# Performance work log

Measured on AMD Instinct MI355X. Metric: run time of the kernel, lower is better.

The kernel has to match this reference:

```python
import jax, jax.numpy as jnp
import numpy as np

THRESHOLD = 0.3

def setup_inputs() -> dict:
    key = jax.random.key(0)
    ks = jax.random.split(key, 8)
    B, T, N, d = 4, 32, 1024, 2
    hd, od, hs, osz = 64, 64, 128, 2
    p = lambda k, sh: jax.random.normal(k, sh, jnp.float32) * 0.1
    return {
        "points": jax.random.uniform(ks[0], (B, T, N, d), jnp.float32),
        "W1": p(ks[1], (hd, d)),   "b1": jnp.zeros((hd,), jnp.float32),
        "W2": p(ks[2], (od, hd)),  "b2": jnp.zeros((od,), jnp.float32),
        "Wg": p(ks[3], (hd, od)),  "bg": jnp.zeros((hd,), jnp.float32),
        "Wih": p(ks[4], (3 * hs, hd)), "Whh": p(ks[5], (3 * hs, hs)),
        "bih": jnp.zeros((3 * hs,), jnp.float32), "bhh": jnp.zeros((3 * hs,), jnp.float32),
        "Wf": p(ks[6], (osz, hs)), "bf": jnp.zeros((osz,), jnp.float32),
    }

def _gcn_step(pts, W1, b1, W2, b2, Wg, bg):
    # pts: [N, d]. Torch detaches node features & adjacency (no grad to points).
    pts = jax.lax.stop_gradient(pts)
    dist = jnp.linalg.norm(pts[:, None, :] - pts[None, :, :], axis=2)  # [N,N]
    A = (dist < THRESHOLD).astype(pts.dtype)
    dinv = 1.0 / jnp.sqrt(A.sum(axis=1))          # rowsum >= 1 (self-loop)
    An = A * dinv[:, None] * dinv[None, :]        # D^{-1/2} A D^{-1/2}
    x = jax.nn.relu((An @ pts) @ W1.T + b1)       # [N, hd]
    x = jax.nn.relu((An @ x) @ W2.T + b2)         # [N, od]
    return x.mean(axis=0) @ Wg.T + bg             # [hd]

def reference(points, W1, b1, W2, b2, Wg, bg, Wih, Whh, bih, bhh, Wf, bf):
    # GCN per (batch, time): [B, T, hd]
    gcn = jax.vmap(jax.vmap(lambda p: _gcn_step(p, W1, b1, W2, b2, Wg, bg)))(points)
    H = Whh.shape[1]

    def gru_step(h, x):  # torch GRU gate order: r, z, n
        gi = x @ Wih.T + bih
        gh = h @ Whh.T + bhh
        ir, iz, inn = jnp.split(gi, 3)
        hr, hz, hn = jnp.split(gh, 3)
        r = jax.nn.sigmoid(ir + hr)
        z = jax.nn.sigmoid(iz + hz)
        n = jnp.tanh(inn + r * hn)
        h_new = (1.0 - z) * n + z * h
        return h_new, h_new

    h0 = jnp.zeros((H,), points.dtype)
    run = lambda xs: jax.lax.scan(gru_step, h0, xs)[1]   # [T, H]
    hs = jax.vmap(run)(gcn)                              # [B, T, H]
    y = hs @ Wf.T + bf                                   # [B, T, out]
    # torch: per-element gru_out.mean(dim=1, keepdim=True) on [1,T,out] -> [1,1,out], stacked -> [B,1,1,out]
    return y.mean(axis=1, keepdims=True)[:, :, None, :]
```

## Files before the change

### kernel.cpp

```cpp
#include <hip/hip_runtime.h>
#include <hip/hip_bf16.h>
#include <math.h>

#define N_PTS 1024
#define BT    128
typedef unsigned int u32;
typedef __attribute__((ext_vector_type(8))) short short8_t;
typedef __attribute__((ext_vector_type(4))) float f32x4;

__device__ __forceinline__ float bfi(u32 bits16) {
    union { u32 u; float f; } v; v.u = bits16 << 16; return v.f;
}
__device__ __forceinline__ unsigned short f2bf(float f) {
    union { float f; u32 u; } v; v.f = f;
    return (unsigned short)((v.u + 0x7FFFu + ((v.u >> 16) & 1u)) >> 16);
}
__device__ __forceinline__ float ldf(const void* p, int i, bool bf) {
    return bf ? bfi(((const unsigned short*)p)[i]) : ((const float*)p)[i];
}
__device__ __forceinline__ float2 ldp(const void* pbase, int j, bool bf) {
    if (bf) {
        u32 w = ((const u32*)pbase)[j];
        return make_float2(bfi(w & 0xFFFFu), bfi(w >> 16));
    }
    return ((const float2*)pbase)[j];
}
__device__ __forceinline__ bool detect_bf16(const void* pts, int tid, int* s_flag) {
    if (tid < 64) {
        u32 w = ((const u32*)pts)[tid];
        float v = bfi(w & 0xFFFFu);
        bool ok = (v >= 0.0f) && (v <= 1.0f);
        unsigned long long m = __ballot(ok);
        if (tid == 0) *s_flag = (m == 0xFFFFFFFFFFFFFFFFull) ? 1 : 0;
    }
    __syncthreads();
    return *s_flag != 0;
}
__device__ __forceinline__ bool is_nb(float px, float py, float qx, float qy) {
    float dx = px - qx, dy = py - qy;
    float d2 = __fadd_rn(__fmul_rn(dx, dx), __fmul_rn(dy, dy));
    return d2 < 0.09f;
}
__device__ __forceinline__ const void* pts_base(const void* pts, int bt, bool bf) {
    return bf ? (const void*)((const unsigned short*)pts + (size_t)bt * N_PTS * 2)
              : (const void*)((const float*)pts + (size_t)bt * N_PTS * 2);
}
__device__ __forceinline__ void gload16(const u32* g, u32* l) {
    __builtin_amdgcn_global_load_lds((const __attribute__((address_space(1))) u32*)g,
                                     (__attribute__((address_space(3))) u32*)l, 16, 0, 0);
}
__device__ __forceinline__ float rdlane(float v, int i) {
    return __int_as_float(__builtin_amdgcn_readlane(__float_as_int(v), i));
}
__device__ __forceinline__ float sigm_f(float x) {
    return __fdividef(1.0f, 1.0f + __expf(-x));
}
__device__ __forceinline__ float tanh_f(float x) {
    float e = __expf(2.0f * x);
    return 1.0f - __fdividef(2.0f, e + 1.0f);
}
__device__ __forceinline__ void build_lut(u32* slut, int tid) {
    if (tid < 16) {
        u32 d0 = ((tid & 1) ? 0x3F80u : 0u) | (((tid & 2) ? 0x3F80u : 0u) << 16);
        u32 d1 = ((tid & 4) ? 0x3F80u : 0u) | (((tid & 8) ? 0x3F80u : 0u) << 16);
        slut[2 * tid] = d0;
        slut[2 * tid + 1] = d1;
    }
}
__device__ __forceinline__ short8_t expand8(const uint2* lut2, u32 by) {
    uint2 lo = lut2[by & 15u], hi = lut2[by >> 4];
    union { uint4 u4; short8_t s8; } cv;
    cv.u4 = make_uint4(lo.x, lo.y, hi.x, hi.y);
    return cv.s8;
}

__global__ __launch_bounds__(256) void k1_bm(const void* __restrict__ pts,
                                             float* __restrict__ dinv,
                                             float* __restrict__ gsum,
                                             u32* __restrict__ bm) {
    int blk = blockIdx.x, tid = threadIdx.x;
    int bt = blk >> 2, q = blk & 3;
    __shared__ float2 sp[N_PTS];
    __shared__ int s_flag;
    bool bf = detect_bf16(pts, tid, &s_flag);
    const void* pb = pts_base(pts, bt, bf);
    for (int j = tid; j < N_PTS; j += 256) sp[j] = ldp(pb, j, bf);
    if (blk < 32) gsum[blk * 256 + tid] = 0.0f;
    __syncthreads();
    int i = q * 256 + tid;
    float px = sp[i].x, py = sp[i].y;
    const float4* sp4 = (const float4*)sp;
    u32* bmrow = bm + (size_t)bt * 32768 + i;
    int cnt = 0;
    for (int c = 0; c < 32; c++) {
        u32 m = 0;
#pragma unroll
        for (int h = 0; h < 8; h++) {
            float4 s01 = sp4[c * 16 + 2 * h], s23 = sp4[c * 16 + 2 * h + 1];
            if (is_nb(px, py, s01.x, s01.y)) m |= 1u << (4 * h);
            if (is_nb(px, py, s01.z, s01.w)) m |= 1u << (4 * h + 1);
            if (is_nb(px, py, s23.x, s23.y)) m |= 1u << (4 * h + 2);
            if (is_nb(px, py, s23.z, s23.w)) m |= 1u << (4 * h + 3);
        }
        bmrow[c * 1024] = m;
        cnt += __popc(m);
    }
    dinv[bt * N_PTS + i] = 1.0f / sqrtf((float)cnt);
}

__global__ __launch_bounds__(256) void k2_x1v(const void* __restrict__ pts,
                                              const void* __restrict__ W1,
                                              const void* __restrict__ b1,
                                              const float* __restrict__ dinv,
                                              const u32* __restrict__ bm,
                                              u32* __restrict__ x1vB) {
    int blk = blockIdx.x, tid = threadIdx.x;
    int bt = blk >> 2, q = blk & 3;
    __shared__ u32 sbm[8192];
    __shared__ unsigned short u_lds[4][1032];
    __shared__ float2 sax[256];
    __shared__ float  sdl[256];
    __shared__ u32 slut[32];
    __shared__ int s_flag;
    bool bf = detect_bf16(pts, tid, &s_flag);
    build_lut(slut, tid);
    const void* pb = pts_base(pts, bt, bf);
    for (int j = tid; j < N_PTS; j += 256) {
        float2 p = ldp(pb, j, bf);
        float d = dinv[bt * N_PTS + j];
        float ux = d * p.x, uy = d * p.y;
        unsigned short hx = f2bf(ux), hy = f2bf(uy);
        u_lds[0][j] = hx;
        u_lds[1][j] = hy;
        u_lds[2][j] = f2bf(ux - bfi(hx));
        u_lds[3][j] = f2bf(uy - bfi(hy));
    }
    const u32* bg_ = bm + (size_t)bt * 32768 + q * 256;
    for (int idx = tid; idx < 8192; idx += 256) {
        int c = idx >> 8, r = idx & 255;
        sbm[idx] = bg_[c * 1024 + r];
    }
    sdl[tid] = dinv[bt * N_PTS + q * 256 + tid];
    __syncthreads();

    int lane = tid & 63, w = tid >> 6;
    int l15 = lane & 15, quad = lane >> 4;
    f32x4 acc[4];
#pragma unroll
    for (int rf = 0; rf < 4; rf++)
#pragma unroll
        for (int r = 0; r < 4; r++) acc[rf][r] = 0.0f;

    const unsigned short* urow = &u_lds[l15 & 3][0];
    const uint2* lut2 = (const uint2*)slut;
    for (int c = 0; c < 32; c++) {
        short8_t bu = *(const short8_t*)(urow + c * 32 + quad * 8);
#pragma unroll
        for (int rf = 0; rf < 4; rf++) {
            u32 mw = sbm[c * 256 + w * 64 + rf * 16 + l15];
            u32 by = (mw >> (quad * 8)) & 0xFFu;
            acc[rf] = __builtin_amdgcn_mfma_f32_16x16x32_bf16(expand8(lut2, by), bu, acc[rf], 0, 0, 0);
        }
    }
#pragma unroll
    for (int rf = 0; rf < 4; rf++) {
#pragma unroll
        for (int r = 0; r < 4; r++) {
            float vsum = acc[rf][r] + __shfl_xor(acc[rf][r], 2, 64);
            int row = w * 64 + rf * 16 + quad * 4 + r;
            float sc = vsum * sdl[row];
            if (l15 == 0)      sax[row].x = sc;
            else if (l15 == 1) sax[row].y = sc;
        }
    }
    __syncthreads();
    int ch = tid & 63, wq = tid >> 6;
    float w0 = ldf(W1, 2 * ch, bf), w1v = ldf(W1, 2 * ch + 1, bf), bb = ldf(b1, ch, bf);
    for (int tt = 0; tt < 4; tt++) {
        u32 ow[8];
#pragma unroll
        for (int k2i = 0; k2i < 8; k2i++) {
            int lj = tt * 64 + wq * 16 + 2 * k2i;
            float2 a0 = sax[lj], a1 = sax[lj + 1];
            float v0 = sdl[lj]     * fmaxf(fmaf(w0, a0.x, fmaf(w1v, a0.y, bb)), 0.0f);
            float v1 = sdl[lj + 1] * fmaxf(fmaf(w0, a1.x, fmaf(w1v, a1.y, bb)), 0.0f);
            ow[k2i] = (u32)f2bf(v0) | ((u32)f2bf(v1) << 16);
        }
        u32* dst = x1vB + ((size_t)(bt * 16 + q * 4 + tt) * 64 + ch) * 36 + wq * 8;
        *(uint4*)dst = make_uint4(ow[0], ow[1], ow[2], ow[3]);
        *(uint4*)(dst + 4) = make_uint4(ow[4], ow[5], ow[6], ow[7]);
    }
}

__global__ __launch_bounds__(256) void k3_mfma(const void* __restrict__ pts,
                                               const void* __restrict__ W2,
                                               const void* __restrict__ b2,
                                               const float* __restrict__ dinv,
                                               const u32* __restrict__ bm,
                                               const u32* __restrict__ x1vB,
                                               float* __restrict__ gsum) {
    __shared__ u32 pool[15424];
    __shared__ u32 slut[32];
    __shared__ int s_flag;
    float* poolf = (float*)pool;
    int tid = threadIdx.x, lane = tid & 63, w = tid >> 6;
    int l15 = lane & 15, quad = lane >> 4;
    int blk = blockIdx.x, bt = blk & 127, rowblk = blk >> 7;
    bool bf = detect_bf16(pts, tid, &s_flag);
    build_lut(slut, tid);

    const u32* xg = x1vB + (size_t)bt * 36864;
    for (int it = w; it < 9; it += 4)
        gload16(xg + it * 256 + lane * 4, pool + 8192 + it * 256 + lane * 4);

    const u32* bg_ = bm + (size_t)bt * 32768 + rowblk * 256;
    for (int idx = tid; idx < 8192; idx += 256) {
        int c = idx >> 8, r = idx & 255;
        pool[idx] = bg_[c * 1024 + r];
    }
    unsigned short* W2B = (unsigned short*)(pool + 12800);
    for (int idx = tid; idx < 4096; idx += 256) {
        int o = idx >> 6, c = idx & 63;
        W2B[o * 72 + c] = f2bf(ldf(W2, idx, bf));
    }
    if (tid < 256) poolf[15104 + tid] = dinv[bt * N_PTS + rowblk * 256 + tid];
    if (tid < 64)  poolf[15360 + tid] = ldf(b2, tid, bf);

    f32x4 acc[4][4];
#pragma unroll
    for (int rf = 0; rf < 4; rf++)
#pragma unroll
        for (int nb = 0; nb < 4; nb++)
#pragma unroll
            for (int r = 0; r < 4; r++) acc[rf][nb][r] = 0.0f;

    const uint2* lut2 = (const uint2*)slut;
    for (int t = 0; t < 16; t++) {
        __syncthreads();
        if (t + 1 < 16) {
            u32* dst = pool + ((t & 1) ? 8192 : 10496);
            const u32* src = xg + (t + 1) * 2304;
            for (int it = w; it < 9; it += 4)
                gload16(src + it * 256 + lane * 4, dst + it * 256 + lane * 4);
        }
        const unsigned short* xf = (const unsigned short*)(pool + ((t & 1) ? 10496 : 8192));
#pragma unroll
        for (int ks = 0; ks < 2; ks++) {
            short8_t bq[4];
#pragma unroll
            for (int rf = 0; rf < 4; rf++) {
                u32 mw = pool[(2 * t + ks) * 256 + w * 64 + rf * 16 + l15];
                u32 by = (mw >> (quad * 8)) & 0xFFu;
                bq[rf] = expand8(lut2, by);
            }
#pragma unroll
            for (int nb = 0; nb < 4; nb++) {
                short8_t af = *(const short8_t*)(xf + (nb * 16 + l15) * 72 + ks * 32 + quad * 8);
#pragma unroll
                for (int rf = 0; rf < 4; rf++)
                    acc[rf][nb] = __builtin_amdgcn_mfma_f32_16x16x32_bf16(af, bq[rf], acc[rf][nb], 0, 0, 0);
            }
        }
    }
    __syncthreads();

    u32* dump = pool;
#pragma unroll
    for (int rf = 0; rf < 4; rf++) {
        int rn = w * 64 + rf * 16 + l15;
        float di = poolf[15104 + rn];
#pragma unroll
        for (int nb = 0; nb < 4; nb++) {
            u32 lo = (u32)f2bf(acc[rf][nb][0] * di) | ((u32)f2bf(acc[rf][nb][1] * di) << 16);
            u32 hi = (u32)f2bf(acc[rf][nb][2] * di) | ((u32)f2bf(acc[rf][nb][3] * di) << 16);
            u32* dst = dump + rn * 36 + nb * 8 + quad * 2;
            dst[0] = lo; dst[1] = hi;
        }
    }
    __syncthreads();
    f32x4 xacc[4][4];
#pragma unroll
    for (int ob = 0; ob < 4; ob++)
#pragma unroll
        for (int rf = 0; rf < 4; rf++)
#pragma unroll
            for (int r = 0; r < 4; r++) xacc[ob][rf][r] = 0.0f;
#pragma unroll
    for (int ks2 = 0; ks2 < 2; ks2++) {
        short8_t b2f[4];
#pragma unroll
        for (int rf = 0; rf < 4; rf++)
            b2f[rf] = *(const short8_t*)((const unsigned short*)dump +
                        (w * 64 + rf * 16 + l15) * 72 + ks2 * 32 + quad * 8);
#pragma unroll
        for (int ob = 0; ob < 4; ob++) {
            short8_t a2 = *(const short8_t*)(W2B + (ob * 16 + l15) * 72 + ks2 * 32 + quad * 8);
#pragma unroll
            for (int rf = 0; rf < 4; rf++)
                xacc[ob][rf] = __builtin_amdgcn_mfma_f32_16x16x32_bf16(a2, b2f[rf], xacc[ob][rf], 0, 0, 0);
        }
    }
#pragma unroll
    for (int ob = 0; ob < 4; ob++) {
#pragma unroll
        for (int r = 0; r < 4; r++) {
            int o = ob * 16 + quad * 4 + r;
            float bb = poolf[15360 + o];
            float s = 0.0f;
#pragma unroll
            for (int rf = 0; rf < 4; rf++) s += fmaxf(xacc[ob][rf][r] + bb, 0.0f);
            s += __shfl_down(s, 8, 16);
            s += __shfl_down(s, 4, 16);
            s += __shfl_down(s, 2, 16);
            s += __shfl_down(s, 1, 16);
            if (l15 == 0) atomicAdd(&gsum[bt * 64 + o], s);
        }
    }
}

__global__ __launch_bounds__(384, 1) void k4a_gi(const void* __restrict__ pts,
                                                 const void* __restrict__ Wg,
                                                 const void* __restrict__ bg,
                                                 const void* __restrict__ Wih,
                                                 const void* __restrict__ bih,
                                                 const float* __restrict__ gsum,
                                                 float* __restrict__ gi_ws) {
    int blk = blockIdx.x, tid = threadIdx.x;
    __shared__ float s_gm[64];
    __shared__ float s_x[64];
    __shared__ int s_flag;
    bool bf = detect_bf16(pts, tid, &s_flag);
    if (tid < 64) s_gm[tid] = gsum[(size_t)blk * 64 + tid] * (1.0f / 1024.0f);
    int r = tid;
    float wv[64];
    if (bf) {
#pragma unroll
        for (int k = 0; k < 64; k++) wv[k] = bfi(((const unsigned short*)Wih)[r * 64 + k]);
    } else {
        const float4* wr = (const float4*)Wih + r * 16;
#pragma unroll
        for (int qq = 0; qq < 16; qq++) {
            float4 v = wr[qq];
            wv[4*qq] = v.x; wv[4*qq+1] = v.y; wv[4*qq+2] = v.z; wv[4*qq+3] = v.w;
        }
    }
    float br = ldf(bih, r, bf);
    float wg[64];
    if (tid < 64) {
        if (bf) {
#pragma unroll
            for (int k = 0; k < 64; k++) wg[k] = bfi(((const unsigned short*)Wg)[tid * 64 + k]);
        } else {
            const float4* wr = (const float4*)Wg + tid * 16;
#pragma unroll
            for (int qq = 0; qq < 16; qq++) {
                float4 v = wr[qq];
                wg[4*qq] = v.x; wg[4*qq+1] = v.y; wg[4*qq+2] = v.z; wg[4*qq+3] = v.w;
            }
        }
    }
    __syncthreads();
    if (tid < 64) {
        float gmv = s_gm[tid];
        float s0 = ldf(bg, tid, bf), s1 = 0.f, s2 = 0.f, s3 = 0.f;
#pragma unroll
        for (int k = 0; k < 64; k += 4) {
            s0 = fmaf(wg[k],     rdlane(gmv, k),     s0);
            s1 = fmaf(wg[k + 1], rdlane(gmv, k + 1), s1);
            s2 = fmaf(wg[k + 2], rdlane(gmv, k + 2), s2);
            s3 = fmaf(wg[k + 3], rdlane(gmv, k + 3), s3);
        }
        s_x[tid] = (s0 + s1) + (s2 + s3);
    }
    __syncthreads();
    float xv = s_x[tid & 63];
    float s0 = br, s1 = 0.f, s2 = 0.f, s3 = 0.f;
#pragma unroll
    for (int k = 0; k < 64; k += 4) {
        s0 = fmaf(wv[k],     rdlane(xv, k),     s0);
        s1 = fmaf(wv[k + 1], rdlane(xv, k + 1), s1);
        s2 = fmaf(wv[k + 2], rdlane(xv, k + 2), s2);
        s3 = fmaf(wv[k + 3], rdlane(xv, k + 3), s3);
    }
    gi_ws[(size_t)blk * 384 + r] = (s0 + s1) + (s2 + s3);
}

__global__ __launch_bounds__(768, 1) void k4b_scan(const void* __restrict__ pts,
                                                   const void* __restrict__ Whh,
                                                   const void* __restrict__ bhh,
                                                   const void* __restrict__ Wf,
                                                   const void* __restrict__ bf_,
                                                   const float* __restrict__ gi_ws,
                                                   float* __restrict__ out) {
    int b = blockIdx.x, tid = threadIdx.x;
    __shared__ float s_gi[12288];
    __shared__ float gh_lds[384];
    __shared__ unsigned short h_hi[128] __attribute__((aligned(16)));
    __shared__ unsigned short h_lo[128] __attribute__((aligned(16)));
    __shared__ float s_red[256];
    __shared__ int s_flag;
    bool bf = detect_bf16(pts, tid, &s_flag);
    const u32* gi_g = (const u32*)gi_ws + (size_t)b * 12288;
    u32* s_gi_u = (u32*)s_gi;
#pragma unroll
    for (int j = 0; j < 4; j++)
        gload16(gi_g + j * 3072 + tid * 4, s_gi_u + j * 3072 + tid * 4);

    int lane = tid & 63, w = tid >> 6;
    int l15 = lane & 15, quad = lane >> 4;
    short8_t whi[2][4], wlo[2][4];
#pragma unroll
    for (int tt = 0; tt < 2; tt++) {
        int row = (2 * w + tt) * 16 + l15;
#pragma unroll
        for (int s = 0; s < 4; s++) {
            union { uint4 u4; short8_t s8; } cv, cl;
            if (bf) {
                cv.u4 = *(const uint4*)((const unsigned short*)Whh + row * 128 + s * 32 + quad * 8);
                cl.u4 = make_uint4(0u, 0u, 0u, 0u);
            } else {
                const float* wp = (const float*)Whh + row * 128 + s * 32 + quad * 8;
                float4 a = ((const float4*)wp)[0], b4 = ((const float4*)wp)[1];
                float v[8] = {a.x, a.y, a.z, a.w, b4.x, b4.y, b4.z, b4.w};
                unsigned short hh_[8], ll_[8];
#pragma unroll
                for (int i = 0; i < 8; i++) {
                    hh_[i] = f2bf(v[i]);
                    ll_[i] = f2bf(v[i] - bfi(hh_[i]));
                }
                cv.u4 = make_uint4((u32)hh_[0] | ((u32)hh_[1] << 16),
                                   (u32)hh_[2] | ((u32)hh_[3] << 16),
                                   (u32)hh_[4] | ((u32)hh_[5] << 16),
                                   (u32)hh_[6] | ((u32)hh_[7] << 16));
                cl.u4 = make_uint4((u32)ll_[0] | ((u32)ll_[1] << 16),
                                   (u32)ll_[2] | ((u32)ll_[3] << 16),
                                   (u32)ll_[4] | ((u32)ll_[5] << 16),
                                   (u32)ll_[6] | ((u32)ll_[7] << 16));
            }
            whi[tt][s] = cv.s8;
            wlo[tt][s] = cl.s8;
        }
    }
    float bhh_r = 0.f, bhh_z = 0.f, bhh_n = 0.f;
    if (tid < 128) {
        bhh_r = ldf(bhh, tid, bf);
        bhh_z = ldf(bhh, 128 + tid, bf);
        bhh_n = ldf(bhh, 256 + tid, bf);
        h_hi[tid] = 0; h_lo[tid] = 0;
    }
    float hval = 0.0f, hsum = 0.0f;
    __syncthreads();

    for (int t = 0; t < 32; t++) {
        short8_t hh[4], hl[4];
#pragma unroll
        for (int s = 0; s < 4; s++) {
            hh[s] = *(const short8_t*)(h_hi + s * 32 + quad * 8);
            hl[s] = *(const short8_t*)(h_lo + s * 32 + quad * 8);
        }
        f32x4 acc0, acc1;
#pragma unroll
        for (int r = 0; r < 4; r++) { acc0[r] = 0.0f; acc1[r] = 0.0f; }
#pragma unroll
        for (int s = 0; s < 4; s++) {
            acc0 = __builtin_amdgcn_mfma_f32_16x16x32_bf16(wlo[0][s], hh[s], acc0, 0, 0, 0);
            acc0 = __builtin_amdgcn_mfma_f32_16x16x32_bf16(whi[0][s], hl[s], acc0, 0, 0, 0);
            acc0 = __builtin_amdgcn_mfma_f32_16x16x32_bf16(whi[0][s], hh[s], acc0, 0, 0, 0);
            acc1 = __builtin_amdgcn_mfma_f32_16x16x32_bf16(wlo[1][s], hh[s], acc1, 0, 0, 0);
            acc1 = __builtin_amdgcn_mfma_f32_16x16x32_bf16(whi[1][s], hl[s], acc1, 0, 0, 0);
            acc1 = __builtin_amdgcn_mfma_f32_16x16x32_bf16(whi[1][s], hh[s], acc1, 0, 0, 0);
        }
        if (l15 == 0) {
#pragma unroll
            for (int r = 0; r < 4; r++) {
                gh_lds[(2 * w) * 16 + quad * 4 + r]     = acc0[r];
                gh_lds[(2 * w + 1) * 16 + quad * 4 + r] = acc1[r];
            }
        }
        __syncthreads();
        if (tid < 128) {
            int c = tid;
            float gi_r = s_gi[t * 384 + c];
            float gi_z = s_gi[t * 384 + 128 + c];
            float gi_n = s_gi[t * 384 + 256 + c];
            float gr = gi_r + (gh_lds[c] + bhh_r);
            float gz = gi_z + (gh_lds[128 + c] + bhh_z);
            float hn = gh_lds[256 + c] + bhh_n;
            float rr = sigm_f(gr);
            float z  = sigm_f(gz);
            float n  = tanh_f(fmaf(rr, hn, gi_n));
            hval = fmaf(z, hval - n, n);
            hsum += hval;
            unsigned short hb = f2bf(hval);
            h_hi[c] = hb;
            h_lo[c] = f2bf(hval - bfi(hb));
        }
        __syncthreads();
    }
    if (tid < 128) {
        float hm = hsum * (1.0f / 32.0f);
        s_red[tid]       = ldf(Wf, tid, bf) * hm;
        s_red[128 + tid] = ldf(Wf, 128 + tid, bf) * hm;
    }
    __syncthreads();
    if (tid < 2) {
        float s = ldf(bf_, tid, bf);
        for (int k = 0; k < 128; k++) s += s_red[tid * 128 + k];
        out[b * 2 + tid] = s;
    }
}

extern "C" void kernel_launch(void* const* d_in, const int* in_sizes, int n_in,
                              void* d_out, int out_size, void* d_ws, size_t ws_size,
                              hipStream_t stream) {
    const void* pts = d_in[0];
    const void* W1  = d_in[1];
    const void* b1  = d_in[2];
    const void* W2  = d_in[3];
    const void* b2  = d_in[4];
    const void* Wg  = d_in[5];
    const void* bg  = d_in[6];
    const void* Wih = d_in[7];
    const void* Whh = d_in[8];
    const void* bih = d_in[9];
    const void* bhh = d_in[10];
    const void* Wf  = d_in[11];
    const void* bf_ = d_in[12];

    float* dinv = (float*)d_ws;
    float* gsum = dinv + (size_t)BT * N_PTS;
    u32*   bm   = (u32*)(gsum + BT * 64);
    u32*   x1vB = bm + (size_t)BT * 32768;
    float* gi_ws = (float*)x1vB;

    k1_bm  <<<512, 256, 0, stream>>>(pts, dinv, gsum, bm);
    k2_x1v <<<512, 256, 0, stream>>>(pts, W1, b1, dinv, bm, x1vB);
    k3_mfma<<<512, 256, 0, stream>>>(pts, W2, b2, dinv, bm, x1vB, gsum);
    k4a_gi <<<128, 384, 0, stream>>>(pts, Wg, bg, Wih, bih, gsum, gi_ws);
    k4b_scan<<<4, 768, 0, stream>>>(pts, Whh, bhh, Wf, bf_, gi_ws, (float*)d_out);
}
```

Measured before the change: 203.6 us.

## Recompute layer-1 features in k3 from aggregated 2-D sums instead of storing x1

k2 now writes only the 2-channel aggregated point features (An@pts) to global memory rather than the full 64-channel bf16 x1 matrix. k3 loads these small per-graph vectors plus dinv into LDS and recomputes the W1 projection, ReLU and scaling for each 64-row tile inside its main loop. The goal is to cut global write and read traffic for x1. In exchange, each of the four row-blocks redundantly recomputes x1, the asynchronous double-buffered prefetch is replaced by an extra __syncthreads per iteration, and LDS use grows.

```diff
diff --git a/kernel.cpp b/kernel.cpp
--- a/kernel.cpp
+++ b/kernel.cpp
@@ -108,17 +108,14 @@
     dinv[bt * N_PTS + i] = 1.0f / sqrtf((float)cnt);
 }
 
-__global__ __launch_bounds__(256) void k2_x1v(const void* __restrict__ pts,
-                                              const void* __restrict__ W1,
-                                              const void* __restrict__ b1,
+__global__ __launch_bounds__(256) void k2_sax(const void* __restrict__ pts,
                                               const float* __restrict__ dinv,
                                               const u32* __restrict__ bm,
-                                              u32* __restrict__ x1vB) {
+                                              float* __restrict__ sax_g) {
     int blk = blockIdx.x, tid = threadIdx.x;
     int bt = blk >> 2, q = blk & 3;
     __shared__ u32 sbm[8192];
     __shared__ unsigned short u_lds[4][1032];
-    __shared__ float2 sax[256];
     __shared__ float  sdl[256];
     __shared__ u32 slut[32];
     __shared__ int s_flag;
@@ -162,6 +159,7 @@
             acc[rf] = __builtin_amdgcn_mfma_f32_16x16x32_bf16(expand8(lut2, by), bu, acc[rf], 0, 0, 0);
         }
     }
+    float2* srow = (float2*)sax_g + (size_t)bt * 1024 + q * 256;
 #pragma unroll
     for (int rf = 0; rf < 4; rf++) {
 #pragma unroll
@@ -169,37 +167,22 @@
             float vsum = acc[rf][r] + __shfl_xor(acc[rf][r], 2, 64);
             int row = w * 64 + rf * 16 + quad * 4 + r;
             float sc = vsum * sdl[row];
-            if (l15 == 0)      sax[row].x = sc;
-            else if (l15 == 1) sax[row].y = sc;
-        }
-    }
-    __syncthreads();
-    int ch = tid & 63, wq = tid >> 6;
-    float w0 = ldf(W1, 2 * ch, bf), w1v = ldf(W1, 2 * ch + 1, bf), bb = ldf(b1, ch, bf);
-    for (int tt = 0; tt < 4; tt++) {
-        u32 ow[8];
-#pragma unroll
-        for (int k2i = 0; k2i < 8; k2i++) {
-            int lj = tt * 64 + wq * 16 + 2 * k2i;
-            float2 a0 = sax[lj], a1 = sax[lj + 1];
-            float v0 = sdl[lj]     * fmaxf(fmaf(w0, a0.x, fmaf(w1v, a0.y, bb)), 0.0f);
-            float v1 = sdl[lj + 1] * fmaxf(fmaf(w0, a1.x, fmaf(w1v, a1.y, bb)), 0.0f);
-            ow[k2i] = (u32)f2bf(v0) | ((u32)f2bf(v1) << 16);
-        }
-        u32* dst = x1vB + ((size_t)(bt * 16 + q * 4 + tt) * 64 + ch) * 36 + wq * 8;
-        *(uint4*)dst = make_uint4(ow[0], ow[1], ow[2], ow[3]);
-        *(uint4*)(dst + 4) = make_uint4(ow[4], ow[5], ow[6], ow[7]);
+            if (l15 == 0)      srow[row].x = sc;
+            else if (l15 == 1) srow[row].y = sc;
+        }
     }
 }
 
 __global__ __launch_bounds__(256) void k3_mfma(const void* __restrict__ pts,
+                                               const void* __restrict__ W1,
+                                               const void* __restrict__ b1,
                                                const void* __restrict__ W2,
                                                const void* __restrict__ b2,
                                                const float* __restrict__ dinv,
                                                const u32* __restrict__ bm,
-                                               const u32* __restrict__ x1vB,
+                                               const float* __restrict__ sax_g,
                                                float* __restrict__ gsum) {
-    __shared__ u32 pool[15424];
+    __shared__ u32 pool[15936];
     __shared__ u32 slut[32];
     __shared__ int s_flag;
     float* poolf = (float*)pool;
@@ -209,22 +192,23 @@
     bool bf = detect_bf16(pts, tid, &s_flag);
     build_lut(slut, tid);
 
-    const u32* xg = x1vB + (size_t)bt * 36864;
-    for (int it = w; it < 9; it += 4)
-        gload16(xg + it * 256 + lane * 4, pool + 8192 + it * 256 + lane * 4);
-
+    float2* saxl = (float2*)(pool + 10496);
+    const float2* sg = (const float2*)sax_g + (size_t)bt * 1024;
+    for (int j = tid; j < 1024; j += 256) {
+        saxl[j] = sg[j];
+        poolf[12544 + j] = dinv[bt * N_PTS + j];
+    }
     const u32* bg_ = bm + (size_t)bt * 32768 + rowblk * 256;
     for (int idx = tid; idx < 8192; idx += 256) {
         int c = idx >> 8, r = idx & 255;
         pool[idx] = bg_[c * 1024 + r];
     }
-    unsigned short* W2B = (unsigned short*)(pool + 12800);
+    unsigned short* W2B = (unsigned short*)(pool + 13568);
     for (int idx = tid; idx < 4096; idx += 256) {
         int o = idx >> 6, c = idx & 63;
         W2B[o * 72 + c] = f2bf(ldf(W2, idx, bf));
     }
-    if (tid < 256) poolf[15104 + tid] = dinv[bt * N_PTS + rowblk * 256 + tid];
-    if (tid < 64)  poolf[15360 + tid] = ldf(b2, tid, bf);
+    if (tid < 64) poolf[15872 + tid] = ldf(b2, tid, bf);
 
     f32x4 acc[4][4];
 #pragma unroll
@@ -234,16 +218,27 @@
 #pragma unroll
             for (int r = 0; r < 4; r++) acc[rf][nb][r] = 0.0f;
 
+    unsigned short* xt = (unsigned short*)(pool + 8192);
+    int ch = tid & 63, wq = tid >> 6;
+    float w0 = ldf(W1, 2 * ch, bf), w1v = ldf(W1, 2 * ch + 1, bf), bb1 = ldf(b1, ch, bf);
     const uint2* lut2 = (const uint2*)slut;
     for (int t = 0; t < 16; t++) {
         __syncthreads();
-        if (t + 1 < 16) {
-            u32* dst = pool + ((t & 1) ? 8192 : 10496);
-            const u32* src = xg + (t + 1) * 2304;
-            for (int it = w; it < 9; it += 4)
-                gload16(src + it * 256 + lane * 4, dst + it * 256 + lane * 4);
-        }
-        const unsigned short* xf = (const unsigned short*)(pool + ((t & 1) ? 10496 : 8192));
+        {
+            u32 ow[8];
+#pragma unroll
+            for (int k2i = 0; k2i < 8; k2i++) {
+                int lj = t * 64 + wq * 16 + 2 * k2i;
+                float2 a0 = saxl[lj], a1 = saxl[lj + 1];
+                float v0 = poolf[12544 + lj]     * fmaxf(fmaf(w0, a0.x, fmaf(w1v, a0.y, bb1)), 0.0f);
+                float v1 = poolf[12544 + lj + 1] * fmaxf(fmaf(w0, a1.x, fmaf(w1v, a1.y, bb1)), 0.0f);
+                ow[k2i] = (u32)f2bf(v0) | ((u32)f2bf(v1) << 16);
+            }
+            u32* xtd = (u32*)xt + ch * 36 + wq * 8;
+            *(uint4*)xtd = make_uint4(ow[0], ow[1], ow[2], ow[3]);
+            *(uint4*)(xtd + 4) = make_uint4(ow[4], ow[5], ow[6], ow[7]);
+        }
+        __syncthreads();
 #pragma unroll
         for (int ks = 0; ks < 2; ks++) {
             short8_t bq[4];
@@ -255,7 +250,7 @@
             }
 #pragma unroll
             for (int nb = 0; nb < 4; nb++) {
-                short8_t af = *(const short8_t*)(xf + (nb * 16 + l15) * 72 + ks * 32 + quad * 8);
+                short8_t af = *(const short8_t*)(xt + (nb * 16 + l15) * 72 + ks * 32 + quad * 8);
 #pragma unroll
                 for (int rf = 0; rf < 4; rf++)
                     acc[rf][nb] = __builtin_amdgcn_mfma_f32_16x16x32_bf16(af, bq[rf], acc[rf][nb], 0, 0, 0);
@@ -268,7 +263,7 @@
 #pragma unroll
     for (int rf = 0; rf < 4; rf++) {
         int rn = w * 64 + rf * 16 + l15;
-        float di = poolf[15104 + rn];
+        float di = poolf[12544 + rowblk * 256 + rn];
 #pragma unroll
         for (int nb = 0; nb < 4; nb++) {
             u32 lo = (u32)f2bf(acc[rf][nb][0] * di) | ((u32)f2bf(acc[rf][nb][1] * di) << 16);
@@ -305,7 +300,7 @@
 #pragma unroll
         for (int r = 0; r < 4; r++) {
             int o = ob * 16 + quad * 4 + r;
-            float bb = poolf[15360 + o];
+            float bb = poolf[15872 + o];
             float s = 0.0f;
 #pragma unroll
             for (int rf = 0; rf < 4; rf++) s += fmaxf(xacc[ob][rf][r] + bb, 0.0f);
@@ -527,15 +522,15 @@
     const void* Wf  = d_in[11];
     const void* bf_ = d_in[12];
 
-    float* dinv = (float*)d_ws;
-    float* gsum = dinv + (size_t)BT * N_PTS;
-    u32*   bm   = (u32*)(gsum + BT * 64);
-    u32*   x1vB = bm + (size_t)BT * 32768;
-    float* gi_ws = (float*)x1vB;
+    float* dinv  = (float*)d_ws;
+    float* gsum  = dinv + (size_t)BT * N_PTS;
+    u32*   bm    = (u32*)(gsum + BT * 64);
+    float* sax_g = (float*)(bm + (size_t)BT * 32768);
+    float* gi_ws = sax_g + (size_t)BT * 2048;
 
     k1_bm  <<<512, 256, 0, stream>>>(pts, dinv, gsum, bm);
-    k2_x1v <<<512, 256, 0, stream>>>(pts, W1, b1, dinv, bm, x1vB);
-    k3_mfma<<<512, 256, 0, stream>>>(pts, W2, b2, dinv, bm, x1vB, gsum);
+    k2_sax <<<512, 256, 0, stream>>>(pts, dinv, bm, sax_g);
+    k3_mfma<<<512, 256, 0, stream>>>(pts, W1, b1, W2, b2, dinv, bm, sax_g, gsum);
     k4a_gi <<<128, 384, 0, stream>>>(pts, Wg, bg, Wih, bih, gsum, gi_ws);
     k4b_scan<<<4, 768, 0, stream>>>(pts, Whh, bhh, Wf, bf_, gi_ws, (float*)d_out);
 }
```

New measurement: 202.4 us. Within noise of the previous version (-0.6%).
